# Performance work log

Hardware: AMD Instinct MI355X
Metric: run time of the kernel (lower is better)

Reference implementation:

```python
import jax, jax.numpy as jnp
import numpy as np


def setup_inputs() -> dict:
    key = jax.random.key(0)
    k1, k2, k3, k4 = jax.random.split(key, 4)
    B, N, M, D = 8, 2048, 2048, 256
    x = jax.random.normal(k1, (B, N, D), dtype=jnp.float32)
    Fi = jax.random.normal(k2, (B, M, D), dtype=jnp.float32)
    # nn.Linear(dim, dim) params (W applied as x @ W.T + b); scale like torch default
    bound = 1.0 / np.sqrt(D)
    W = jax.random.uniform(k3, (D, D), dtype=jnp.float32, minval=-bound, maxval=bound)
    b = jax.random.uniform(k4, (D,), dtype=jnp.float32, minval=-bound, maxval=bound)
    return {"x": x, "Fi": Fi, "W": W, "b": b}


def reference(x, Fi, W, b):
    # x: [B, N, D], Fi: [B, M, D]
    q = jnp.einsum("bnd,ed->bne", x, W) + b          # linear projection
    scores = jnp.einsum("bnd,bmd->bnm", q, Fi)        # QK^T (no scaling in original)
    attn = jax.nn.softmax(scores, axis=-1)            # softmax over keys
    out = jnp.einsum("bnm,bmd->bnd", attn, Fi)        # attention @ V (V = Fi)
    return out
```

## Files before the change

### kernel.cpp

```cpp
#include <hip/hip_runtime.h>
#include <hip/hip_bf16.h>

typedef _Float16 half8 __attribute__((ext_vector_type(8)));
typedef float floatx4 __attribute__((ext_vector_type(4)));

#define MFMA16H(a, b, c) __builtin_amdgcn_mfma_f32_16x16x32_f16((a), (b), (c), 0, 0, 0)

static constexpr int Bb = 8, Nn = 2048, Mm = 2048, Dd = 256;

__device__ inline void async16(const void* g, void* l)
{
    __builtin_amdgcn_global_load_lds((const __attribute__((address_space(1))) unsigned int*)g,
                                     (__attribute__((address_space(3))) unsigned int*)l,
                                     16, 0, 0);
}

__device__ inline half8 cvt8h(const float* __restrict__ p)
{
    float4 f0 = *reinterpret_cast<const float4*>(p);
    float4 f1 = *reinterpret_cast<const float4*>(p + 4);
    half8 r;
    r[0] = (_Float16)f0.x; r[1] = (_Float16)f0.y; r[2] = (_Float16)f0.z; r[3] = (_Float16)f0.w;
    r[4] = (_Float16)f1.x; r[5] = (_Float16)f1.y; r[6] = (_Float16)f1.z; r[7] = (_Float16)f1.w;
    return r;
}

__device__ inline void cvt8h_split(const float* __restrict__ p, half8& h, half8& l)
{
    float4 f0 = *reinterpret_cast<const float4*>(p);
    float4 f1 = *reinterpret_cast<const float4*>(p + 4);
    float f[8] = {f0.x, f0.y, f0.z, f0.w, f1.x, f1.y, f1.z, f1.w};
#pragma unroll
    for (int i = 0; i < 8; ++i) {
        _Float16 hh = (_Float16)f[i];
        h[i] = hh;
        l[i] = (_Float16)(f[i] - (float)hh);
    }
}

__global__ __launch_bounds__(256, 4)
void prep_kernel(const float* __restrict__ Fi, const float* __restrict__ W,
                 _Float16* __restrict__ FiH, _Float16* __restrict__ FiT,
                 _Float16* __restrict__ Wh, _Float16* __restrict__ Wl)
{
    const int bid = blockIdx.x;
    const int t = threadIdx.x;

    if (bid >= 1024) {
        const size_t base = (size_t)(bid - 1024) * 2048 + t * 8;
        half8 h, l;
        cvt8h_split(W + base, h, l);
        *(half8*)(Wh + base) = h;
        *(half8*)(Wl + base) = l;
        return;
    }

    __shared__ __align__(16) unsigned short tile[64][64];
    const int b  = bid >> 7;
    const int mt = (bid >> 2) & 31;
    const int dt = bid & 3;
    {
        const int i = t >> 2, jc = (t & 3) * 16;
        const int pc = ((jc >> 4) ^ (i >> 4)) * 16;
        const float* src = Fi + ((size_t)b * Mm + mt * 64 + i) * Dd + dt * 64 + jc;
        union { half8 v; uint4 u; } p0, p1;
        p0.v = cvt8h(src);
        p1.v = cvt8h(src + 8);
        *(uint4*)&tile[i][pc]     = p0.u;
        *(uint4*)&tile[i][pc + 8] = p1.u;
        unsigned short* dh = reinterpret_cast<unsigned short*>(FiH)
            + ((size_t)b * Mm + mt * 64 + i) * Dd + dt * 64 + jc;
        *(uint4*)dh       = p0.u;
        *(uint4*)(dh + 8) = p1.u;
    }
    __syncthreads();
    {
        const int d = t >> 2, mc = (t & 3) * 16;
        unsigned short* dst = reinterpret_cast<unsigned short*>(FiT)
            + ((size_t)b * Dd + dt * 64 + d) * Mm + mt * 64 + mc;
        union { uint4 v[2]; unsigned short s[16]; } u;
#pragma unroll
        for (int s = 0; s < 16; ++s) {
            const int row = mc + s;
            u.s[s] = tile[row][((d >> 4) ^ (row >> 4)) * 16 + (d & 15)];
        }
        *(uint4*)dst       = u.v[0];
        *(uint4*)(dst + 8) = u.v[1];
    }
}

__global__ __launch_bounds__(256, 2)
void qproj_kernel(const float* __restrict__ x, const _Float16* __restrict__ Wh,
                  const _Float16* __restrict__ Wl, const float* __restrict__ bias,
                  _Float16* __restrict__ q)
{
    __shared__ __align__(16) _Float16 sWhA[256 * 32];
    __shared__ __align__(16) _Float16 sWlA[256 * 32];
    __shared__ __align__(16) _Float16 sWhB[256 * 32];
    __shared__ __align__(16) _Float16 sWlB[256 * 32];

    const int tid = threadIdx.x;
    const int lane = tid & 63, w = tid >> 6;
    const int lo = lane & 15, hi = lane >> 4;
    const long r0 = (long)blockIdx.x * 32;

    floatx4 acc[2][4];
#pragma unroll
    for (int rt = 0; rt < 2; ++rt)
#pragma unroll
        for (int j = 0; j < 4; ++j) acc[rt][j] = (floatx4)0.0f;

    const int se = lane >> 2, sc = lane & 3;

    auto stage = [&](int k0, _Float16* dWh, _Float16* dWl) {
#pragma unroll
        for (int j = 0; j < 4; ++j) {
            const int e0 = (w * 4 + j) * 16;
            const int e = e0 + se;
            const int gc = sc ^ (e & 3);
            async16(Wh + (size_t)e * Dd + k0 + gc * 8, dWh + e0 * 32);
            async16(Wl + (size_t)e * Dd + k0 + gc * 8, dWl + e0 * 32);
        }
    };

    auto compute = [&](int k0, const _Float16* SWh, const _Float16* SWl) {
        half8 ah[2], al[2];
#pragma unroll
        for (int rt = 0; rt < 2; ++rt)
            cvt8h_split(x + (size_t)(r0 + rt * 16 + lo) * Dd + k0 + hi * 8, ah[rt], al[rt]);
#pragma unroll
        for (int jj = 0; jj < 4; ++jj) {
            const int e = (w * 4 + jj) * 16 + lo;
            half8 bh = *reinterpret_cast<const half8*>(&SWh[(e & 255) * 32 + ((hi ^ (e & 3)) * 8)]);
            half8 bl = *reinterpret_cast<const half8*>(&SWl[(e & 255) * 32 + ((hi ^ (e & 3)) * 8)]);
#pragma unroll
            for (int rt = 0; rt < 2; ++rt) {
                acc[rt][jj] = MFMA16H(ah[rt], bh, acc[rt][jj]);
                acc[rt][jj] = MFMA16H(ah[rt], bl, acc[rt][jj]);
                acc[rt][jj] = MFMA16H(al[rt], bh, acc[rt][jj]);
            }
        }
    };

    stage(0, sWhA, sWlA);
    for (int k0 = 0; k0 < 256; k0 += 64) {
        __syncthreads();
        stage(k0 + 32, sWhB, sWlB);
        compute(k0, sWhA, sWlA);
        __syncthreads();
        if (k0 + 64 < 256) stage(k0 + 64, sWhA, sWlA);
        compute(k0 + 32, sWhB, sWlB);
    }
#pragma unroll
    for (int jj = 0; jj < 4; ++jj) {
        const int e = (w * 4 + jj) * 16 + lo;
        const float bv = bias[e];
#pragma unroll
        for (int rt = 0; rt < 2; ++rt)
#pragma unroll
            for (int r = 0; r < 4; ++r)
                q[(size_t)(r0 + rt * 16 + hi * 4 + r) * Dd + e] = (_Float16)(acc[rt][jj][r] + bv);
    }
}

__global__ __launch_bounds__(256, 2)
void flash_kernel(const _Float16* __restrict__ q, const _Float16* __restrict__ FiH,
                  const _Float16* __restrict__ FiT, _Float16* __restrict__ o_part,
                  float* __restrict__ m_part, float* __restrict__ l_part)
{
    __shared__ __align__(16) _Float16 sFiA[32 * 256];
    __shared__ __align__(16) _Float16 sFiB[32 * 256];
    __shared__ __align__(16) _Float16 sFiTA[256 * 32];
    __shared__ __align__(16) _Float16 sFiTB[256 * 32];
    __shared__ __align__(16) _Float16 sP[4][32 * 36];

    const int bid = blockIdx.x;
    const int b  = bid & 7;
    const int u  = bid >> 3;
    const int nt = u & 15;
    const int kh = u >> 4;
    const int tid = threadIdx.x;
    const int lane = tid & 63, w = tid >> 6;
    const int lo = lane & 15, hi = lane >> 4;
    const int nbase = nt * 128 + w * 32;

    const _Float16* fH = FiH + (size_t)b * Mm * Dd;
    const _Float16* fT = FiT + (size_t)b * Dd * Mm;

    half8 qf[2][8];
    const _Float16* qb = q + ((size_t)b * Nn + nbase + lo) * Dd + hi * 8;
#pragma unroll
    for (int rt = 0; rt < 2; ++rt)
#pragma unroll
        for (int kk = 0; kk < 8; ++kk)
            qf[rt][kk] = *reinterpret_cast<const half8*>(qb + rt * 16 * Dd + kk * 32);

    half8 ones;
#pragma unroll
    for (int i = 0; i < 8; ++i) ones[i] = (_Float16)1.0f;

    floatx4 o[2][16];
    floatx4 ol[2];
#pragma unroll
    for (int rt = 0; rt < 2; ++rt) {
#pragma unroll
        for (int t = 0; t < 16; ++t) o[rt][t] = (floatx4)0.0f;
        ol[rt] = (floatx4)0.0f;
    }
    float m_i[2][4];
#pragma unroll
    for (int rt = 0; rt < 2; ++rt)
#pragma unroll
        for (int r = 0; r < 4; ++r) m_i[rt][r] = -INFINITY;

    auto stage = [&](int it, _Float16* dFi, _Float16* dFiT) {
        const int key0 = kh * 512 + it * 32;
#pragma unroll
        for (int j = 0; j < 4; ++j) {
            const int rbase = (w * 4 + j) * 2;
            const int r = rbase + (lane >> 5);
            const int gc = (lane & 31) ^ (r & 7);
            async16(fH + (size_t)(key0 + r) * Dd + gc * 8, dFi + rbase * 256);
        }
#pragma unroll
        for (int j = 0; j < 4; ++j) {
            const int rbase = (w + j * 4) * 16;
            const int r = rbase + (lane >> 2);
            const int gc = (lane & 3) ^ (r & 3);
            async16(fT + (size_t)r * Mm + key0 + gc * 8, dFiT + rbase * 32);
        }
    };

    auto compute = [&](const _Float16* SFI, const _Float16* SFIT) {
        floatx4 s[2][2];
#pragma unroll
        for (int rt = 0; rt < 2; ++rt)
#pragma unroll
            for (int st = 0; st < 2; ++st) s[rt][st] = (floatx4)0.0f;
#pragma unroll
        for (int st = 0; st < 2; ++st) {
            const int row = st * 16 + lo;
#pragma unroll
            for (int kk = 0; kk < 8; ++kk) {
                half8 bv = *reinterpret_cast<const half8*>(
                    SFI + row * 256 + (((kk * 4 + hi) ^ (lo & 7)) * 8));
                s[0][st] = MFMA16H(qf[0][kk], bv, s[0][st]);
                s[1][st] = MFMA16H(qf[1][kk], bv, s[1][st]);
            }
        }

        float mn[2][4];
        bool chg = false;
#pragma unroll
        for (int rt = 0; rt < 2; ++rt)
#pragma unroll
            for (int r = 0; r < 4; ++r) {
                float mc = fmaxf(s[rt][0][r], s[rt][1][r]);
                mc = fmaxf(mc, __shfl_xor(mc, 1));
                mc = fmaxf(mc, __shfl_xor(mc, 2));
                mc = fmaxf(mc, __shfl_xor(mc, 4));
                mc = fmaxf(mc, __shfl_xor(mc, 8));
                mn[rt][r] = fmaxf(m_i[rt][r], mc);
                chg = chg || (mn[rt][r] > m_i[rt][r]);
            }
        if (__any(chg)) {
#pragma unroll
            for (int rt = 0; rt < 2; ++rt) {
                float al4[4];
#pragma unroll
                for (int r = 0; r < 4; ++r) {
                    al4[r] = __expf(m_i[rt][r] - mn[rt][r]);
                    m_i[rt][r] = mn[rt][r];
                }
#pragma unroll
                for (int t = 0; t < 16; ++t) {
                    floatx4 ot = o[rt][t];
#pragma unroll
                    for (int r = 0; r < 4; ++r) ot[r] *= al4[r];
                    o[rt][t] = ot;
                }
#pragma unroll
                for (int r = 0; r < 4; ++r) ol[rt][r] *= al4[r];
            }
        }
#pragma unroll
        for (int rt = 0; rt < 2; ++rt)
#pragma unroll
            for (int r = 0; r < 4; ++r) {
                _Float16 p0 = (_Float16)__expf(s[rt][0][r] - m_i[rt][r]);
                _Float16 p1 = (_Float16)__expf(s[rt][1][r] - m_i[rt][r]);
                sP[w][(rt * 16 + hi * 4 + r) * 36 + lo]      = p0;
                sP[w][(rt * 16 + hi * 4 + r) * 36 + 16 + lo] = p1;
            }

        half8 pa0 = *reinterpret_cast<const half8*>(&sP[w][lo * 36 + hi * 8]);
        half8 pa1 = *reinterpret_cast<const half8*>(&sP[w][(16 + lo) * 36 + hi * 8]);
#pragma unroll
        for (int t = 0; t < 16; ++t) {
            half8 bv = *reinterpret_cast<const half8*>(
                SFIT + (t * 16 + lo) * 32 + ((hi ^ (lo & 3)) * 8));
            o[0][t] = MFMA16H(pa0, bv, o[0][t]);
            o[1][t] = MFMA16H(pa1, bv, o[1][t]);
        }
        ol[0] = MFMA16H(pa0, ones, ol[0]);
        ol[1] = MFMA16H(pa1, ones, ol[1]);
    };

    stage(0, sFiA, sFiTA);
    for (int it = 0; it < 16; it += 2) {
        __syncthreads();
        stage(it + 1, sFiB, sFiTB);
        compute(sFiA, sFiTA);
        __syncthreads();
        if (it + 2 < 16) stage(it + 2, sFiA, sFiTA);
        compute(sFiB, sFiTB);
    }

#pragma unroll
    for (int rt = 0; rt < 2; ++rt)
#pragma unroll
        for (int r = 0; r < 4; ++r) {
            const long gq = (long)b * Nn + nbase + rt * 16 + hi * 4 + r;
            const size_t obase = ((size_t)kh * (Bb * Nn) + gq) * Dd;
#pragma unroll
            for (int t = 0; t < 16; ++t)
                o_part[obase + t * 16 + lo] = (_Float16)o[rt][t][r];
            if (lo == 0) {
                m_part[(size_t)kh * (Bb * Nn) + gq] = m_i[rt][r];
                l_part[(size_t)kh * (Bb * Nn) + gq] = ol[rt][r];
            }
        }
}

__global__ __launch_bounds__(256, 8)
void merge_kernel(const _Float16* __restrict__ o_part, const float* __restrict__ m_part,
                  const float* __restrict__ l_part, float* __restrict__ out)
{
    const int col = threadIdx.x;
#pragma unroll
    for (int rr = 0; rr < 8; ++rr) {
        const int row = blockIdx.x * 8 + rr;
        float m[4], l[4];
#pragma unroll
        for (int k = 0; k < 4; ++k) {
            m[k] = m_part[(size_t)k * (Bb * Nn) + row];
            l[k] = l_part[(size_t)k * (Bb * Nn) + row];
        }
        float M = fmaxf(fmaxf(m[0], m[1]), fmaxf(m[2], m[3]));
        float denom = 0.f, acc = 0.f;
#pragma unroll
        for (int k = 0; k < 4; ++k) {
            const float wk = __expf(m[k] - M);
            denom += wk * l[k];
            acc += wk * (float)o_part[((size_t)k * (Bb * Nn) + row) * Dd + col];
        }
        out[(size_t)row * Dd + col] = acc / denom;
    }
}

extern "C" void kernel_launch(void* const* d_in, const int* in_sizes, int n_in,
                              void* d_out, int out_size, void* d_ws, size_t ws_size,
                              hipStream_t stream)
{
    const float* x    = (const float*)d_in[0];
    const float* Fi   = (const float*)d_in[1];
    const float* W    = (const float*)d_in[2];
    const float* bias = (const float*)d_in[3];
    float* out = (float*)d_out;

    _Float16* q_ws = (_Float16*)d_ws;
    _Float16* FiH  = q_ws + (size_t)Bb * Nn * Dd;
    _Float16* FiT  = FiH + (size_t)Bb * Mm * Dd;
    _Float16* Wh   = FiT + (size_t)Bb * Dd * Mm;
    _Float16* Wl   = Wh + (size_t)Dd * Dd;
    _Float16* o_part = Wl + (size_t)Dd * Dd;
    float* m_part  = (float*)(o_part + (size_t)4 * Bb * Nn * Dd);
    float* l_part  = m_part + (size_t)4 * Bb * Nn;

    hipLaunchKernelGGL(prep_kernel, dim3(1056), dim3(256), 0, stream, Fi, W, FiH, FiT, Wh, Wl);
    hipLaunchKernelGGL(qproj_kernel, dim3(512), dim3(256), 0, stream, x, Wh, Wl, bias, q_ws);
    hipLaunchKernelGGL(flash_kernel, dim3(512), dim3(256), 0, stream, q_ws, FiH, FiT,
                       o_part, m_part, l_part);
    hipLaunchKernelGGL(merge_kernel, dim3(2048), dim3(256), 0, stream, o_part, m_part, l_part, out);
}
```

Baseline: 213.2 us.

## Merge Fi conversion into q-projection launch and add lazy softmax rescale threshold

Splits the W hi/lo conversion into its own small kernel, then merges the Fi fp16 convert/transpose blocks and the q-projection blocks into one launch so the two independent jobs can share the GPU at the same time. The Fi path now uses the larger shared buffer sized for the projection, which may lower occupancy for those blocks. Separately, the flash kernel now rescales the running output only when the row max rises by more than 4, which skips many rescale passes. The stale max stays correct because it is still used consistently for exp and the final normalisation, with some added risk of exp overflow headroom.

```diff
diff --git a/kernel.cpp b/kernel.cpp
--- a/kernel.cpp
+++ b/kernel.cpp
@@ -38,71 +38,74 @@
     }
 }
 
-__global__ __launch_bounds__(256, 4)
-void prep_kernel(const float* __restrict__ Fi, const float* __restrict__ W,
-                 _Float16* __restrict__ FiH, _Float16* __restrict__ FiT,
-                 _Float16* __restrict__ Wh, _Float16* __restrict__ Wl)
-{
+__global__ __launch_bounds__(256, 8)
+void wsplit_kernel(const float* __restrict__ W,
+                   _Float16* __restrict__ Wh, _Float16* __restrict__ Wl)
+{
+    const size_t base = (size_t)blockIdx.x * 2048 + threadIdx.x * 8;
+    half8 h, l;
+    cvt8h_split(W + base, h, l);
+    *(half8*)(Wh + base) = h;
+    *(half8*)(Wl + base) = l;
+}
+
+__global__ __launch_bounds__(256, 2)
+void prepq_kernel(const float* __restrict__ x, const float* __restrict__ Fi,
+                  const _Float16* __restrict__ Wh, const _Float16* __restrict__ Wl,
+                  const float* __restrict__ bias,
+                  _Float16* __restrict__ FiH, _Float16* __restrict__ FiT,
+                  _Float16* __restrict__ q)
+{
+    __shared__ __align__(16) _Float16 smem[4 * 256 * 32];
     const int bid = blockIdx.x;
     const int t = threadIdx.x;
 
-    if (bid >= 1024) {
-        const size_t base = (size_t)(bid - 1024) * 2048 + t * 8;
-        half8 h, l;
-        cvt8h_split(W + base, h, l);
-        *(half8*)(Wh + base) = h;
-        *(half8*)(Wl + base) = l;
+    if (bid >= 512) {
+        unsigned short (*tile)[64] = reinterpret_cast<unsigned short (*)[64]>(smem);
+        const int pbid = bid - 512;
+        const int b  = pbid >> 7;
+        const int mt = (pbid >> 2) & 31;
+        const int dt = pbid & 3;
+        {
+            const int i = t >> 2, jc = (t & 3) * 16;
+            const int pc = ((jc >> 4) ^ (i >> 4)) * 16;
+            const float* src = Fi + ((size_t)b * Mm + mt * 64 + i) * Dd + dt * 64 + jc;
+            union { half8 v; uint4 u; } p0, p1;
+            p0.v = cvt8h(src);
+            p1.v = cvt8h(src + 8);
+            *(uint4*)&tile[i][pc]     = p0.u;
+            *(uint4*)&tile[i][pc + 8] = p1.u;
+            unsigned short* dh = reinterpret_cast<unsigned short*>(FiH)
+                + ((size_t)b * Mm + mt * 64 + i) * Dd + dt * 64 + jc;
+            *(uint4*)dh       = p0.u;
+            *(uint4*)(dh + 8) = p1.u;
+        }
+        __syncthreads();
+        {
+            const int d = t >> 2, mc = (t & 3) * 16;
+            unsigned short* dst = reinterpret_cast<unsigned short*>(FiT)
+                + ((size_t)b * Dd + dt * 64 + d) * Mm + mt * 64 + mc;
+            union { uint4 v[2]; unsigned short s[16]; } u;
+#pragma unroll
+            for (int s = 0; s < 16; ++s) {
+                const int row = mc + s;
+                u.s[s] = tile[row][((d >> 4) ^ (row >> 4)) * 16 + (d & 15)];
+            }
+            *(uint4*)dst       = u.v[0];
+            *(uint4*)(dst + 8) = u.v[1];
+        }
         return;
     }
 
-    __shared__ __align__(16) unsigned short tile[64][64];
-    const int b  = bid >> 7;
-    const int mt = (bid >> 2) & 31;
-    const int dt = bid & 3;
-    {
-        const int i = t >> 2, jc = (t & 3) * 16;
-        const int pc = ((jc >> 4) ^ (i >> 4)) * 16;
-        const float* src = Fi + ((size_t)b * Mm + mt * 64 + i) * Dd + dt * 64 + jc;
-        union { half8 v; uint4 u; } p0, p1;
-        p0.v = cvt8h(src);
-        p1.v = cvt8h(src + 8);
-        *(uint4*)&tile[i][pc]     = p0.u;
-        *(uint4*)&tile[i][pc + 8] = p1.u;
-        unsigned short* dh = reinterpret_cast<unsigned short*>(FiH)
-            + ((size_t)b * Mm + mt * 64 + i) * Dd + dt * 64 + jc;
-        *(uint4*)dh       = p0.u;
-        *(uint4*)(dh + 8) = p1.u;
-    }
-    __syncthreads();
-    {
-        const int d = t >> 2, mc = (t & 3) * 16;
-        unsigned short* dst = reinterpret_cast<unsigned short*>(FiT)
-            + ((size_t)b * Dd + dt * 64 + d) * Mm + mt * 64 + mc;
-        union { uint4 v[2]; unsigned short s[16]; } u;
-#pragma unroll
-        for (int s = 0; s < 16; ++s) {
-            const int row = mc + s;
-            u.s[s] = tile[row][((d >> 4) ^ (row >> 4)) * 16 + (d & 15)];
-        }
-        *(uint4*)dst       = u.v[0];
-        *(uint4*)(dst + 8) = u.v[1];
-    }
-}
-
-__global__ __launch_bounds__(256, 2)
-void qproj_kernel(const float* __restrict__ x, const _Float16* __restrict__ Wh,
-                  const _Float16* __restrict__ Wl, const float* __restrict__ bias,
-                  _Float16* __restrict__ q)
-{
-    __shared__ __align__(16) _Float16 sWhA[256 * 32];
-    __shared__ __align__(16) _Float16 sWlA[256 * 32];
-    __shared__ __align__(16) _Float16 sWhB[256 * 32];
-    __shared__ __align__(16) _Float16 sWlB[256 * 32];
-
-    const int tid = threadIdx.x;
+    _Float16* sWhA = smem;
+    _Float16* sWlA = smem + 256 * 32;
+    _Float16* sWhB = smem + 2 * 256 * 32;
+    _Float16* sWlB = smem + 3 * 256 * 32;
+
+    const int tid = t;
     const int lane = tid & 63, w = tid >> 6;
     const int lo = lane & 15, hi = lane >> 4;
-    const long r0 = (long)blockIdx.x * 32;
+    const long r0 = (long)bid * 32;
 
     floatx4 acc[2][4];
 #pragma unroll
@@ -261,7 +264,7 @@
                 mc = fmaxf(mc, __shfl_xor(mc, 4));
                 mc = fmaxf(mc, __shfl_xor(mc, 8));
                 mn[rt][r] = fmaxf(m_i[rt][r], mc);
-                chg = chg || (mn[rt][r] > m_i[rt][r]);
+                chg = chg || (mn[rt][r] > m_i[rt][r] + 4.0f);
             }
         if (__any(chg)) {
 #pragma unroll
@@ -377,8 +380,9 @@
     float* m_part  = (float*)(o_part + (size_t)4 * Bb * Nn * Dd);
     float* l_part  = m_part + (size_t)4 * Bb * Nn;
 
-    hipLaunchKernelGGL(prep_kernel, dim3(1056), dim3(256), 0, stream, Fi, W, FiH, FiT, Wh, Wl);
-    hipLaunchKernelGGL(qproj_kernel, dim3(512), dim3(256), 0, stream, x, Wh, Wl, bias, q_ws);
+    hipLaunchKernelGGL(wsplit_kernel, dim3(32), dim3(256), 0, stream, W, Wh, Wl);
+    hipLaunchKernelGGL(prepq_kernel, dim3(1536), dim3(256), 0, stream,
+                       x, Fi, Wh, Wl, bias, FiH, FiT, q_ws);
     hipLaunchKernelGGL(flash_kernel, dim3(512), dim3(256), 0, stream, q_ws, FiH, FiT,
                        o_part, m_part, l_part);
     hipLaunchKernelGGL(merge_kernel, dim3(2048), dim3(256), 0, stream, o_part, m_part, l_part, out);
```

After: 357.6 us. 67.7% more time.
